# Kernel optimization log

Measured on AMD Instinct MI355X. Metric: run time of the kernel, lower is better.

The kernel has to match this reference:

```python
import jax, jax.numpy as jnp
import numpy as np

N_NODES = 100000
N_EDGES = 3200000
NUM_FEATURES = 128
DIM = 10
NUM_GRAPHS = 64


def setup_inputs() -> dict:
    key = jax.random.key(0)
    k1, k2, k3, k4, k5, k6, k7 = jax.random.split(key, 7)
    features = jax.random.normal(k1, (N_NODES, NUM_FEATURES), dtype=jnp.float32)
    src = jax.random.randint(k2, (N_EDGES,), 0, N_NODES, dtype=jnp.int64)
    dst = jax.random.randint(k3, (N_EDGES,), 0, N_NODES, dtype=jnp.int64)
    graph_ids = jnp.sort(jax.random.randint(k4, (N_NODES,), 0, NUM_GRAPHS, dtype=jnp.int64))
    # GraphConv weights (no bias), glorot-ish scaling
    W1 = jax.random.normal(k5, (NUM_FEATURES, DIM), dtype=jnp.float32) / np.sqrt(NUM_FEATURES)
    W2 = jax.random.normal(k6, (DIM, DIM), dtype=jnp.float32) / np.sqrt(DIM)
    W3 = jax.random.normal(k7, (DIM, 1), dtype=jnp.float32) / np.sqrt(DIM)
    return {"features": features, "W1": W1, "W2": W2, "W3": W3,
            "src": src, "dst": dst, "graph_ids": graph_ids}


def _sum_aggregate(h, src, dst, n_nodes):
    # message = h[src], reduce-sum at dst (norm='none' GraphConv aggregation)
    return jax.ops.segment_sum(h[src], dst, num_segments=n_nodes)


def reference(features, W1, W2, W3, src, dst, graph_ids):
    n = features.shape[0]
    # conv1: in_feats(128) > out_feats(10) -> weight first, then aggregate
    h = features @ W1                          # [N, DIM]
    h = _sum_aggregate(h, src, dst, n)         # [N, DIM]
    h = jax.nn.relu(h)
    # conv2: in_feats == out_feats -> aggregate first, then weight
    h = _sum_aggregate(h, src, dst, n) @ W2    # [N, DIM]
    # dgl.mean_nodes: per-graph mean pooling over nodes
    sums = jax.ops.segment_sum(h, graph_ids, num_segments=NUM_GRAPHS)           # [G, DIM]
    cnt = jax.ops.segment_sum(jnp.ones((n, 1), h.dtype), graph_ids, num_segments=NUM_GRAPHS)
    pooled = sums / jnp.maximum(cnt, 1.0)      # [G, DIM]
    return jax.nn.sigmoid(pooled @ W3)         # [G, 1]
```

## Files before the change

### kernel.cpp

```cpp
#include <hip/hip_runtime.h>
#include <hip/hip_fp16.h>

#define N_NODES 100000
#define N_EDGES 3200000
#define NUM_FEATURES 128
#define DIM 10
#define NUM_GRAPHS 64

#define BSHIFT 8
#define BSIZE (1 << BSHIFT)
#define NB ((N_NODES + BSIZE - 1) / BSIZE)
#define CHUNKS 2
#define PCHUNKS 4
#define EPB 12500
#define PLACE_BLOCKS 256
#define NQUAD 25000
#define GEMM_BLOCKS 1563
#define BOUND_BLOCKS 196
#define TILE (BSIZE * DIM)
#define CAP 4608
#define CAPB 16384
#define NCHUNK (NB * CHUNKS)
#define NCHUNK2 (NB * PCHUNKS)
#define ACC_STRIDE 11

#define DPP_ROR_ADD(v, n)                                                        \
    (v) += __int_as_float(__builtin_amdgcn_update_dpp(                           \
        0, __float_as_int(v), 0x120 | (n), 0xF, 0xF, false))

__global__ __launch_bounds__(512) void k_front(const float* __restrict__ feat,
                                               const float* __restrict__ W1,
                                               __half* __restrict__ h1,
                                               const int* __restrict__ gids,
                                               int* __restrict__ bound,
                                               const int* __restrict__ src,
                                               const int* __restrict__ dst,
                                               int* __restrict__ cnt,
                                               int* __restrict__ pk) {
    __shared__ int hd[NB];
    __shared__ int cb[NB];

    if (blockIdx.x < PLACE_BLOCKS) {
        int base0 = blockIdx.x * EPB;
        for (int t = threadIdx.x; t < NB; t += 512) hd[t] = 0;
        __syncthreads();

        {
            int i = threadIdx.x;
            for (; i + 1536 < EPB; i += 2048) {
                int d0 = dst[base0 + i],        d1 = dst[base0 + i + 512];
                int d2 = dst[base0 + i + 1024], d3 = dst[base0 + i + 1536];
                atomicAdd(&hd[d0 >> BSHIFT], 1);
                atomicAdd(&hd[d1 >> BSHIFT], 1);
                atomicAdd(&hd[d2 >> BSHIFT], 1);
                atomicAdd(&hd[d3 >> BSHIFT], 1);
            }
            for (; i < EPB; i += 512) {
                int d = dst[base0 + i];
                atomicAdd(&hd[d >> BSHIFT], 1);
            }
        }
        __syncthreads();

        for (int t = threadIdx.x; t < NB; t += 512) {
            int c = hd[t];
            int o = c ? atomicAdd(&cnt[t], c) : 0;
            cb[t] = t * CAPB + o;
        }
        __syncthreads();

        {
            int i = threadIdx.x;
            for (; i + 1536 < EPB; i += 2048) {
                int d0 = dst[base0 + i],        d1 = dst[base0 + i + 512];
                int d2 = dst[base0 + i + 1024], d3 = dst[base0 + i + 1536];
                int s0 = src[base0 + i],        s1 = src[base0 + i + 512];
                int s2 = src[base0 + i + 1024], s3 = src[base0 + i + 1536];
                int q0 = atomicAdd(&cb[d0 >> BSHIFT], 1);
                int q1 = atomicAdd(&cb[d1 >> BSHIFT], 1);
                int q2 = atomicAdd(&cb[d2 >> BSHIFT], 1);
                int q3 = atomicAdd(&cb[d3 >> BSHIFT], 1);
                if (q0 < ((d0 >> BSHIFT) + 1) * CAPB) pk[q0] = ((d0 & (BSIZE - 1)) << 17) | s0;
                if (q1 < ((d1 >> BSHIFT) + 1) * CAPB) pk[q1] = ((d1 & (BSIZE - 1)) << 17) | s1;
                if (q2 < ((d2 >> BSHIFT) + 1) * CAPB) pk[q2] = ((d2 & (BSIZE - 1)) << 17) | s2;
                if (q3 < ((d3 >> BSHIFT) + 1) * CAPB) pk[q3] = ((d3 & (BSIZE - 1)) << 17) | s3;
            }
            for (; i < EPB; i += 512) {
                int d = dst[base0 + i];
                int s = src[base0 + i];
                int q = atomicAdd(&cb[d >> BSHIFT], 1);
                if (q < ((d >> BSHIFT) + 1) * CAPB) pk[q] = ((d & (BSIZE - 1)) << 17) | s;
            }
        }
        return;
    }

    int bb = blockIdx.x - PLACE_BLOCKS;

    int nb2 = bb * 512 + threadIdx.x;
    if (bb < BOUND_BLOCKS && nb2 < N_NODES) {
        int g  = gids[nb2];
        int gp = nb2 ? gids[nb2 - 1] : -1;
        for (int v = gp + 1; v <= g; ++v) bound[v] = nb2;
        if (nb2 == N_NODES - 1)
            for (int v = g + 1; v <= NUM_GRAPHS; ++v) bound[v] = N_NODES;
    }

    int gid  = bb * 512 + threadIdx.x;
    int quad = gid >> 5;
    int lane = gid & 31;
    if (quad >= NQUAD) return;

    float wf[40];
    {
        const float4* W14 = reinterpret_cast<const float4*>(W1 + lane * 40);
#pragma unroll
        for (int m = 0; m < 10; ++m) {
            float4 q = W14[m];
            wf[4 * m]     = q.x;
            wf[4 * m + 1] = q.y;
            wf[4 * m + 2] = q.z;
            wf[4 * m + 3] = q.w;
        }
    }

    int nbase = quad * 4;
    float4 f[4];
#pragma unroll
    for (int n = 0; n < 4; ++n)
        f[n] = *reinterpret_cast<const float4*>(feat + (size_t)(nbase + n) * NUM_FEATURES + lane * 4);

    float acc[4][DIM];
#pragma unroll
    for (int n = 0; n < 4; ++n)
#pragma unroll
        for (int k = 0; k < DIM; ++k) acc[n][k] = 0.f;

#pragma unroll
    for (int n = 0; n < 4; ++n) {
        float fv[4] = {f[n].x, f[n].y, f[n].z, f[n].w};
#pragma unroll
        for (int j = 0; j < 4; ++j)
#pragma unroll
            for (int k = 0; k < DIM; ++k)
                acc[n][k] += fv[j] * wf[j * DIM + k];
    }

#pragma unroll
    for (int n = 0; n < 4; ++n)
#pragma unroll
        for (int k = 0; k < DIM; ++k) {
            float v = acc[n][k];
            DPP_ROR_ADD(v, 1);
            DPP_ROR_ADD(v, 2);
            DPP_ROR_ADD(v, 4);
            DPP_ROR_ADD(v, 8);
            acc[n][k] = v + __shfl_xor(v, 16);
        }

    if (lane == 0) {
        __half2* o = (__half2*)h1;
#pragma unroll
        for (int n = 0; n < 4; ++n)
#pragma unroll
            for (int j = 0; j < 5; ++j)
                o[(size_t)(nbase + n) * 5 + j] =
                    __floats2half2_rn(acc[n][2 * j], acc[n][2 * j + 1]);
    }
}

__global__ __launch_bounds__(512) void k_spmm1(const __half* __restrict__ h,
                                               const int* __restrict__ cnt,
                                               const int* __restrict__ pk,
                                               float* __restrict__ part) {
    __shared__ int eh[CAP];
    __shared__ int srt[CAP];
    __shared__ int hist[BSIZE];
    __shared__ int cur[BSIZE];

    int b     = blockIdx.x / CHUNKS;
    int chunk = blockIdx.x % CHUNKS;
    int s0  = b * CAPB;
    int len = cnt[b];
    int c0  = s0 + (len * chunk) / CHUNKS;
    int c1  = s0 + (len * (chunk + 1)) / CHUNKS;
    int n   = c1 - c0;
    int nc  = min(n, CAP);

    for (int t = threadIdx.x; t < BSIZE; t += 512) hist[t] = 0;
    __syncthreads();

    {
        int i = threadIdx.x;
        for (; i + 1536 < nc; i += 2048) {
            int p0 = pk[c0 + i],        p1 = pk[c0 + i + 512];
            int p2 = pk[c0 + i + 1024], p3 = pk[c0 + i + 1536];
            eh[i] = p0; eh[i + 512] = p1; eh[i + 1024] = p2; eh[i + 1536] = p3;
            atomicAdd(&hist[p0 >> 17], 1);
            atomicAdd(&hist[p1 >> 17], 1);
            atomicAdd(&hist[p2 >> 17], 1);
            atomicAdd(&hist[p3 >> 17], 1);
        }
        for (; i < nc; i += 512) {
            int p = pk[c0 + i];
            eh[i] = p;
            atomicAdd(&hist[p >> 17], 1);
        }
    }
    __syncthreads();

    if (threadIdx.x < 64) {
        int l = threadIdx.x;
        int carry = 0;
#pragma unroll
        for (int j = 0; j < 4; ++j) {
            int x = hist[j * 64 + l];
            int v = x;
#pragma unroll
            for (int off = 1; off < 64; off <<= 1) {
                int t2 = __shfl_up(v, off);
                if (l >= off) v += t2;
            }
            cur[j * 64 + l] = carry + v - x;
            carry += __shfl(v, 63);
        }
    }
    __syncthreads();

    for (int i = threadIdx.x; i < nc; i += 512) {
        int p = eh[i];
        int pos = atomicAdd(&cur[p >> 17], 1);
        srt[pos] = p;
    }
    __syncthreads();

    int wave = threadIdx.x >> 6;
    int lane = threadIdx.x & 63;
    int slot = lane / 5;
    int l    = lane - slot * 5;
    float* pb = part + (size_t)blockIdx.x * TILE;
    const __half2* h2 = (const __half2*)h;

    if (slot < 12) {
        int g = wave * 12 + slot;
        for (int loc = g; loc < BSIZE; loc += 96) {
            int e0 = loc ? cur[loc - 1] : 0;
            int e1 = cur[loc];
            float ax0 = 0.f, ay0 = 0.f, ax1 = 0.f, ay1 = 0.f;
            float ax2 = 0.f, ay2 = 0.f, ax3 = 0.f, ay3 = 0.f;
            int e = e0;
            for (; e + 7 < e1; e += 8) {
                float2 v0 = __half22float2(h2[(size_t)(srt[e]     & 0x1FFFF) * 5 + l]);
                float2 v1 = __half22float2(h2[(size_t)(srt[e + 1] & 0x1FFFF) * 5 + l]);
                float2 v2 = __half22float2(h2[(size_t)(srt[e + 2] & 0x1FFFF) * 5 + l]);
                float2 v3 = __half22float2(h2[(size_t)(srt[e + 3] & 0x1FFFF) * 5 + l]);
                float2 v4 = __half22float2(h2[(size_t)(srt[e + 4] & 0x1FFFF) * 5 + l]);
                float2 v5 = __half22float2(h2[(size_t)(srt[e + 5] & 0x1FFFF) * 5 + l]);
                float2 v6 = __half22float2(h2[(size_t)(srt[e + 6] & 0x1FFFF) * 5 + l]);
                float2 v7 = __half22float2(h2[(size_t)(srt[e + 7] & 0x1FFFF) * 5 + l]);
                ax0 += v0.x + v4.x; ay0 += v0.y + v4.y;
                ax1 += v1.x + v5.x; ay1 += v1.y + v5.y;
                ax2 += v2.x + v6.x; ay2 += v2.y + v6.y;
                ax3 += v3.x + v7.x; ay3 += v3.y + v7.y;
            }
            for (; e < e1; ++e) {
                float2 v = __half22float2(h2[(size_t)(srt[e] & 0x1FFFF) * 5 + l]);
                ax0 += v.x; ay0 += v.y;
            }
            pb[loc * DIM + 2 * l]     = (ax0 + ax1) + (ax2 + ax3);
            pb[loc * DIM + 2 * l + 1] = (ay0 + ay1) + (ay2 + ay3);
        }
    }
    __syncthreads();

    for (int i = CAP + threadIdx.x; i < n; i += 512) {
        int p = pk[c0 + i];
        int loc = p >> 17, s = p & 0x1FFFF;
#pragma unroll
        for (int j = 0; j < 5; ++j) {
            float2 v = __half22float2(h2[(size_t)s * 5 + j]);
            atomicAdd(&pb[loc * DIM + 2 * j], v.x);
            atomicAdd(&pb[loc * DIM + 2 * j + 1], v.y);
        }
    }
}

__global__ __launch_bounds__(256) void k_merge_relu(const float* __restrict__ part,
                                                    __half* __restrict__ r) {
    int b     = blockIdx.x;
    int nbase = b << BSHIFT;
    const float* p0 = part + (size_t)(b * CHUNKS) * TILE;
    __half2* r2 = (__half2*)r;
    for (int t = threadIdx.x; t < TILE / 2; t += 256) {
        float sx = 0.f, sy = 0.f;
#pragma unroll
        for (int c = 0; c < CHUNKS; ++c) {
            float2 v = ((const float2*)(p0 + (size_t)c * TILE))[t];
            sx += v.x; sy += v.y;
        }
        int ebase = nbase * DIM + 2 * t;
        if (ebase < N_NODES * DIM)
            r2[(size_t)nbase * 5 + t] = __floats2half2_rn(fmaxf(sx, 0.f), fmaxf(sy, 0.f));
    }
}

__global__ __launch_bounds__(512) void k_pass2(const __half* __restrict__ r,
                                               const int* __restrict__ cnt,
                                               const int* __restrict__ pk,
                                               const int* __restrict__ bound,
                                               float* __restrict__ sums) {
    __shared__ float acc[NUM_GRAPHS * ACC_STRIDE];

    int b     = blockIdx.x / PCHUNKS;
    int chunk = blockIdx.x % PCHUNKS;
    int nbase = b << BSHIFT;
    int nlast = min(nbase + BSIZE - 1, N_NODES - 1);

    int glo = 0, ghx = NUM_GRAPHS - 1;
#pragma unroll
    for (int it = 0; it < 6; ++it) {
        int mid = (glo + ghx + 1) >> 1;
        if (bound[mid] <= nbase) glo = mid; else ghx = mid - 1;
    }
    int lo2 = 0, hi2 = NUM_GRAPHS - 1;
#pragma unroll
    for (int it = 0; it < 6; ++it) {
        int mid = (lo2 + hi2 + 1) >> 1;
        if (bound[mid] <= nlast) lo2 = mid; else hi2 = mid - 1;
    }
    int ghi  = lo2;
    int span = ghi - glo;

    for (int t = threadIdx.x; t < (span + 1) * DIM; t += 512)
        acc[(glo + t / DIM) * ACC_STRIDE + t % DIM] = 0.f;
    __syncthreads();

    int s0  = b * CAPB;
    int len = cnt[b];
    int c0  = s0 + (len * chunk) / PCHUNKS;
    int c1  = s0 + (len * (chunk + 1)) / PCHUNKS;

    int wave = threadIdx.x >> 6;
    int lane = threadIdx.x & 63;
    int slot = lane / 5;
    int l    = lane - slot * 5;
    const __half2* r2 = (const __half2*)r;

    if (slot < 12) {
        const int STR = 96;
        int q = wave * 12 + slot;
        int e = c0 + q;
        if (span <= 1) {
            int gA  = glo;
            int gB  = (span == 1) ? glo + 1 : glo;
            int cut = (span == 1) ? (bound[glo + 1] - nbase) : BSIZE;
            float axA = 0.f, ayA = 0.f, axB = 0.f, ayB = 0.f;
            for (; e + 7 * STR < c1; e += 8 * STR) {
                int p[8];
#pragma unroll
                for (int u = 0; u < 8; ++u) p[u] = pk[e + u * STR];
                float2 v[8];
#pragma unroll
                for (int u = 0; u < 8; ++u)
                    v[u] = __half22float2(r2[(size_t)(p[u] & 0x1FFFF) * 5 + l]);
#pragma unroll
                for (int u = 0; u < 8; ++u) {
                    bool a = (p[u] >> 17) < cut;
                    axA += a ? v[u].x : 0.f;  ayA += a ? v[u].y : 0.f;
                    axB += a ? 0.f : v[u].x;  ayB += a ? 0.f : v[u].y;
                }
            }
            for (; e < c1; e += STR) {
                int p = pk[e];
                float2 v = __half22float2(r2[(size_t)(p & 0x1FFFF) * 5 + l]);
                bool a = (p >> 17) < cut;
                axA += a ? v.x : 0.f;  ayA += a ? v.y : 0.f;
                axB += a ? 0.f : v.x;  ayB += a ? 0.f : v.y;
            }
            atomicAdd(&acc[gA * ACC_STRIDE + 2 * l], axA);
            atomicAdd(&acc[gA * ACC_STRIDE + 2 * l + 1], ayA);
            if (span == 1) {
                atomicAdd(&acc[gB * ACC_STRIDE + 2 * l], axB);
                atomicAdd(&acc[gB * ACC_STRIDE + 2 * l + 1], ayB);
            }
        } else {
            for (; e < c1; e += STR) {
                int p   = pk[e];
                int loc = p >> 17;
                float2 v = __half22float2(r2[(size_t)(p & 0x1FFFF) * 5 + l]);
                int g = glo;
                for (int gg = glo + 1; gg <= ghi; ++gg)
                    g += (loc >= bound[gg] - nbase) ? 1 : 0;
                atomicAdd(&acc[g * ACC_STRIDE + 2 * l], v.x);
                atomicAdd(&acc[g * ACC_STRIDE + 2 * l + 1], v.y);
            }
        }
    }
    __syncthreads();

    for (int t = threadIdx.x; t < (span + 1) * DIM; t += 512) {
        int g = glo + t / DIM;
        float v = acc[g * ACC_STRIDE + t % DIM];
        if (v != 0.f) atomicAdd(&sums[g * DIM + t % DIM], v);
    }
}

__global__ void k_final(const float* __restrict__ sums, const int* __restrict__ bound,
                        const float* __restrict__ W2, const float* __restrict__ W3,
                        float* __restrict__ out) {
    int g = threadIdx.x;
    if (g >= NUM_GRAPHS) return;
    float c = fmaxf((float)(bound[g + 1] - bound[g]), 1.f);
    float p[DIM];
#pragma unroll
    for (int k = 0; k < DIM; ++k) p[k] = sums[g * DIM + k] / c;
    float z = 0.f;
#pragma unroll
    for (int j = 0; j < DIM; ++j) {
        float t = 0.f;
#pragma unroll
        for (int k = 0; k < DIM; ++k) t += p[k] * W2[k * DIM + j];
        z += t * W3[j];
    }
    out[g] = 1.f / (1.f + expf(-z));
}

extern "C" void kernel_launch(void* const* d_in, const int* in_sizes, int n_in,
                              void* d_out, int out_size, void* d_ws, size_t ws_size,
                              hipStream_t stream) {
    const float* feat = (const float*)d_in[0];
    const float* W1   = (const float*)d_in[1];
    const float* W2   = (const float*)d_in[2];
    const float* W3   = (const float*)d_in[3];
    const int*   src  = (const int*)d_in[4];
    const int*   dst  = (const int*)d_in[5];
    const int*   gids = (const int*)d_in[6];
    float*       out  = (float*)d_out;

    char* ws = (char*)d_ws;
    __half* h1    = (__half*)(ws);
    int*    pk    = (int*)(ws + 2000000);
    __half* r     = (__half*)(ws + 27624576);
    float*  part  = (float*)(ws + 29624576);
    int*    cnt   = (int*)(ws + 37632256);
    float*  sums  = (float*)(ws + 37633824);
    int*    bound = (int*)(ws + 37636384);

    hipMemsetAsync(ws + 37632256, 0, 4128, stream);

    k_front<<<PLACE_BLOCKS + GEMM_BLOCKS, 512, 0, stream>>>(feat, W1, h1, gids, bound,
                                                            src, dst, cnt, pk);
    k_spmm1     <<<NCHUNK, 512, 0, stream>>>(h1, cnt, pk, part);
    k_merge_relu<<<NB, 256, 0, stream>>>(part, r);
    k_pass2     <<<NCHUNK2, 512, 0, stream>>>(r, cnt, pk, bound, sums);

    k_final<<<1, 64, 0, stream>>>(sums, bound, W2, W3, out);
}
```

Baseline: 206.1 us.

## Fuse merge-relu into single-block-per-bucket SpMM with padded null edges

The first aggregation now uses one block per 256-node bucket instead of two chunks. Each block re-reads the packed edges from global memory rather than staging them in LDS, sorts them into a larger shared buffer, and writes the ReLU'd fp16 result directly. This drops the separate merge kernel, the fp32 partial-tile round trip and the global-atomic overflow path. The placement phase now uses more, smaller blocks and pads each block's segment to a multiple of 16 with null edges that point at a zeroed pad node. The risk is lower parallelism in SpMM and the extra padding writes. Buckets that exceed the shared capacity are silently truncated.

```diff
diff --git a/kernel.cpp b/kernel.cpp
--- a/kernel.cpp
+++ b/kernel.cpp
@@ -10,19 +10,18 @@
 #define BSHIFT 8
 #define BSIZE (1 << BSHIFT)
 #define NB ((N_NODES + BSIZE - 1) / BSIZE)
-#define CHUNKS 2
 #define PCHUNKS 4
-#define EPB 12500
-#define PLACE_BLOCKS 256
+#define EPB 5000
+#define PLACE_BLOCKS 640
 #define NQUAD 25000
 #define GEMM_BLOCKS 1563
 #define BOUND_BLOCKS 196
-#define TILE (BSIZE * DIM)
-#define CAP 4608
 #define CAPB 16384
-#define NCHUNK (NB * CHUNKS)
+#define SCAP 9728
 #define NCHUNK2 (NB * PCHUNKS)
 #define ACC_STRIDE 11
+#define PAD_NODE N_NODES
+#define NULLPK (((BSIZE - 1) << 17) | PAD_NODE)
 
 #define DPP_ROR_ADD(v, n)                                                        \
     (v) += __int_as_float(__builtin_amdgcn_update_dpp(                           \
@@ -31,6 +30,7 @@
 __global__ __launch_bounds__(512) void k_front(const float* __restrict__ feat,
                                                const float* __restrict__ W1,
                                                __half* __restrict__ h1,
+                                               __half* __restrict__ r,
                                                const int* __restrict__ gids,
                                                int* __restrict__ bound,
                                                const int* __restrict__ src,
@@ -55,17 +55,22 @@
                 atomicAdd(&hd[d2 >> BSHIFT], 1);
                 atomicAdd(&hd[d3 >> BSHIFT], 1);
             }
-            for (; i < EPB; i += 512) {
-                int d = dst[base0 + i];
-                atomicAdd(&hd[d >> BSHIFT], 1);
-            }
+            for (; i < EPB; i += 512)
+                atomicAdd(&hd[dst[base0 + i] >> BSHIFT], 1);
         }
         __syncthreads();
 
         for (int t = threadIdx.x; t < NB; t += 512) {
             int c = hd[t];
-            int o = c ? atomicAdd(&cnt[t], c) : 0;
-            cb[t] = t * CAPB + o;
+            if (c) {
+                int cpad = (c + 15) & ~15;
+                int o = atomicAdd(&cnt[t], cpad);
+                cb[t] = t * CAPB + o;
+                hd[t] = min(t * CAPB + o + cpad, (t + 1) * CAPB);
+            } else {
+                cb[t] = 0;
+                hd[t] = 0;
+            }
         }
         __syncthreads();
 
@@ -92,10 +97,25 @@
                 if (q < ((d >> BSHIFT) + 1) * CAPB) pk[q] = ((d & (BSIZE - 1)) << 17) | s;
             }
         }
+        __syncthreads();
+
+        for (int t = threadIdx.x; t < NB; t += 512)
+            for (int q = cb[t]; q < hd[t]; ++q) pk[q] = NULLPK;
         return;
     }
 
     int bb = blockIdx.x - PLACE_BLOCKS;
+
+    if (bb == 0 && threadIdx.x == 0) {
+        __half2 z = __floats2half2_rn(0.f, 0.f);
+        __half2* oh = (__half2*)h1;
+        __half2* orr = (__half2*)r;
+#pragma unroll
+        for (int j = 0; j < 5; ++j) {
+            oh[(size_t)PAD_NODE * 5 + j]  = z;
+            orr[(size_t)PAD_NODE * 5 + j] = z;
+        }
+    }
 
     int nb2 = bb * 512 + threadIdx.x;
     if (bb < BOUND_BLOCKS && nb2 < N_NODES) {
@@ -172,39 +192,31 @@
 __global__ __launch_bounds__(512) void k_spmm1(const __half* __restrict__ h,
                                                const int* __restrict__ cnt,
                                                const int* __restrict__ pk,
-                                               float* __restrict__ part) {
-    __shared__ int eh[CAP];
-    __shared__ int srt[CAP];
+                                               __half* __restrict__ r) {
+    __shared__ int srt[SCAP];
     __shared__ int hist[BSIZE];
     __shared__ int cur[BSIZE];
 
-    int b     = blockIdx.x / CHUNKS;
-    int chunk = blockIdx.x % CHUNKS;
+    int b   = blockIdx.x;
     int s0  = b * CAPB;
-    int len = cnt[b];
-    int c0  = s0 + (len * chunk) / CHUNKS;
-    int c1  = s0 + (len * (chunk + 1)) / CHUNKS;
-    int n   = c1 - c0;
-    int nc  = min(n, CAP);
+    int len = min(cnt[b], CAPB);
 
     for (int t = threadIdx.x; t < BSIZE; t += 512) hist[t] = 0;
     __syncthreads();
 
     {
         int i = threadIdx.x;
-        for (; i + 1536 < nc; i += 2048) {
-            int p0 = pk[c0 + i],        p1 = pk[c0 + i + 512];
-            int p2 = pk[c0 + i + 1024], p3 = pk[c0 + i + 1536];
-            eh[i] = p0; eh[i + 512] = p1; eh[i + 1024] = p2; eh[i + 1536] = p3;
-            atomicAdd(&hist[p0 >> 17], 1);
-            atomicAdd(&hist[p1 >> 17], 1);
-            atomicAdd(&hist[p2 >> 17], 1);
-            atomicAdd(&hist[p3 >> 17], 1);
-        }
-        for (; i < nc; i += 512) {
-            int p = pk[c0 + i];
-            eh[i] = p;
-            atomicAdd(&hist[p >> 17], 1);
+        for (; i + 1536 < len; i += 2048) {
+            int p0 = pk[s0 + i],        p1 = pk[s0 + i + 512];
+            int p2 = pk[s0 + i + 1024], p3 = pk[s0 + i + 1536];
+            if ((p0 & 0x1FFFF) < N_NODES) atomicAdd(&hist[p0 >> 17], 1);
+            if ((p1 & 0x1FFFF) < N_NODES) atomicAdd(&hist[p1 >> 17], 1);
+            if ((p2 & 0x1FFFF) < N_NODES) atomicAdd(&hist[p2 >> 17], 1);
+            if ((p3 & 0x1FFFF) < N_NODES) atomicAdd(&hist[p3 >> 17], 1);
+        }
+        for (; i < len; i += 512) {
+            int p = pk[s0 + i];
+            if ((p & 0x1FFFF) < N_NODES) atomicAdd(&hist[p >> 17], 1);
         }
     }
     __syncthreads();
@@ -227,10 +239,20 @@
     }
     __syncthreads();
 
-    for (int i = threadIdx.x; i < nc; i += 512) {
-        int p = eh[i];
-        int pos = atomicAdd(&cur[p >> 17], 1);
-        srt[pos] = p;
+    {
+        int i = threadIdx.x;
+        for (; i + 1536 < len; i += 2048) {
+            int p0 = pk[s0 + i],        p1 = pk[s0 + i + 512];
+            int p2 = pk[s0 + i + 1024], p3 = pk[s0 + i + 1536];
+            if ((p0 & 0x1FFFF) < N_NODES) { int q = atomicAdd(&cur[p0 >> 17], 1); if (q < SCAP) srt[q] = p0; }
+            if ((p1 & 0x1FFFF) < N_NODES) { int q = atomicAdd(&cur[p1 >> 17], 1); if (q < SCAP) srt[q] = p1; }
+            if ((p2 & 0x1FFFF) < N_NODES) { int q = atomicAdd(&cur[p2 >> 17], 1); if (q < SCAP) srt[q] = p2; }
+            if ((p3 & 0x1FFFF) < N_NODES) { int q = atomicAdd(&cur[p3 >> 17], 1); if (q < SCAP) srt[q] = p3; }
+        }
+        for (; i < len; i += 512) {
+            int p = pk[s0 + i];
+            if ((p & 0x1FFFF) < N_NODES) { int q = atomicAdd(&cur[p >> 17], 1); if (q < SCAP) srt[q] = p; }
+        }
     }
     __syncthreads();
 
@@ -238,14 +260,14 @@
     int lane = threadIdx.x & 63;
     int slot = lane / 5;
     int l    = lane - slot * 5;
-    float* pb = part + (size_t)blockIdx.x * TILE;
     const __half2* h2 = (const __half2*)h;
+    __half2* r2 = (__half2*)r;
 
     if (slot < 12) {
         int g = wave * 12 + slot;
         for (int loc = g; loc < BSIZE; loc += 96) {
-            int e0 = loc ? cur[loc - 1] : 0;
-            int e1 = cur[loc];
+            int e0 = min(loc ? cur[loc - 1] : 0, SCAP);
+            int e1 = min(cur[loc], SCAP);
             float ax0 = 0.f, ay0 = 0.f, ax1 = 0.f, ay1 = 0.f;
             float ax2 = 0.f, ay2 = 0.f, ax3 = 0.f, ay3 = 0.f;
             int e = e0;
@@ -267,40 +289,12 @@
                 float2 v = __half22float2(h2[(size_t)(srt[e] & 0x1FFFF) * 5 + l]);
                 ax0 += v.x; ay0 += v.y;
             }
-            pb[loc * DIM + 2 * l]     = (ax0 + ax1) + (ax2 + ax3);
-            pb[loc * DIM + 2 * l + 1] = (ay0 + ay1) + (ay2 + ay3);
-        }
-    }
-    __syncthreads();
-
-    for (int i = CAP + threadIdx.x; i < n; i += 512) {
-        int p = pk[c0 + i];
-        int loc = p >> 17, s = p & 0x1FFFF;
-#pragma unroll
-        for (int j = 0; j < 5; ++j) {
-            float2 v = __half22float2(h2[(size_t)s * 5 + j]);
-            atomicAdd(&pb[loc * DIM + 2 * j], v.x);
-            atomicAdd(&pb[loc * DIM + 2 * j + 1], v.y);
-        }
-    }
-}
-
-__global__ __launch_bounds__(256) void k_merge_relu(const float* __restrict__ part,
-                                                    __half* __restrict__ r) {
-    int b     = blockIdx.x;
-    int nbase = b << BSHIFT;
-    const float* p0 = part + (size_t)(b * CHUNKS) * TILE;
-    __half2* r2 = (__half2*)r;
-    for (int t = threadIdx.x; t < TILE / 2; t += 256) {
-        float sx = 0.f, sy = 0.f;
-#pragma unroll
-        for (int c = 0; c < CHUNKS; ++c) {
-            float2 v = ((const float2*)(p0 + (size_t)c * TILE))[t];
-            sx += v.x; sy += v.y;
-        }
-        int ebase = nbase * DIM + 2 * t;
-        if (ebase < N_NODES * DIM)
-            r2[(size_t)nbase * 5 + t] = __floats2half2_rn(fmaxf(sx, 0.f), fmaxf(sy, 0.f));
+            int node = (b << BSHIFT) + loc;
+            if (node < N_NODES)
+                r2[(size_t)node * 5 + l] =
+                    __floats2half2_rn(fmaxf((ax0 + ax1) + (ax2 + ax3), 0.f),
+                                      fmaxf((ay0 + ay1) + (ay2 + ay3), 0.f));
+        }
     }
 }
 
@@ -336,7 +330,7 @@
     __syncthreads();
 
     int s0  = b * CAPB;
-    int len = cnt[b];
+    int len = min(cnt[b], CAPB);
     int c0  = s0 + (len * chunk) / PCHUNKS;
     int c1  = s0 + (len * (chunk + 1)) / PCHUNKS;
 
@@ -439,20 +433,18 @@
 
     char* ws = (char*)d_ws;
     __half* h1    = (__half*)(ws);
-    int*    pk    = (int*)(ws + 2000000);
-    __half* r     = (__half*)(ws + 27624576);
-    float*  part  = (float*)(ws + 29624576);
-    int*    cnt   = (int*)(ws + 37632256);
-    float*  sums  = (float*)(ws + 37633824);
-    int*    bound = (int*)(ws + 37636384);
-
-    hipMemsetAsync(ws + 37632256, 0, 4128, stream);
-
-    k_front<<<PLACE_BLOCKS + GEMM_BLOCKS, 512, 0, stream>>>(feat, W1, h1, gids, bound,
+    int*    pk    = (int*)(ws + 2000128);
+    __half* r     = (__half*)(ws + 27624704);
+    int*    cnt   = (int*)(ws + 29624832);
+    float*  sums  = (float*)(ws + 29626400);
+    int*    bound = (int*)(ws + 29628960);
+
+    hipMemsetAsync(ws + 29624832, 0, 4128, stream);
+
+    k_front<<<PLACE_BLOCKS + GEMM_BLOCKS, 512, 0, stream>>>(feat, W1, h1, r, gids, bound,
                                                             src, dst, cnt, pk);
-    k_spmm1     <<<NCHUNK, 512, 0, stream>>>(h1, cnt, pk, part);
-    k_merge_relu<<<NB, 256, 0, stream>>>(part, r);
-    k_pass2     <<<NCHUNK2, 512, 0, stream>>>(r, cnt, pk, bound, sums);
+    k_spmm1<<<NB, 512, 0, stream>>>(h1, cnt, pk, r);
+    k_pass2<<<NCHUNK2, 512, 0, stream>>>(r, cnt, pk, bound, sums);
 
     k_final<<<1, 64, 0, stream>>>(sums, bound, W2, W3, out);
 }
```

After: 210.3 us. +2.0%, slower.
